# Optimization experiments

Measured on AMD Instinct MI355X. Metric: run time of the kernel, lower is better.

## Reference

```python
import jax, jax.numpy as jnp
import numpy as np

NEG_INF = -1e9  # matches torch masked_fill(-1000000000.0)


def setup_inputs() -> dict:
    key = jax.random.key(0)
    kv, kk, kq, km, kw, kb = jax.random.split(key, 6)
    B, Lq, Lk, D = 8, 1024, 4096, 1024  # Lq must equal D (transpose-then-merge quirk)
    v = jax.random.normal(kv, (B, Lk, D), dtype=jnp.float32)
    k = jax.random.normal(kk, (B, Lk, D), dtype=jnp.float32)
    q = jax.random.normal(kq, (B, Lq, D), dtype=jnp.float32)
    mask = jax.random.randint(km, (B, Lq, Lk), 0, 2) > 0  # bool, True = masked out
    W_merge = jax.random.normal(kw, (D, D), dtype=jnp.float32) / np.sqrt(D)
    b_merge = jax.random.normal(kb, (D,), dtype=jnp.float32) * 0.02
    return {"v": v, "k": k, "q": q, "mask": mask, "W_merge": W_merge, "b_merge": b_merge}


def reference(v, k, q, mask, W_merge, b_merge):
    d_k = q.shape[-1]
    scale = 1.0 / jnp.sqrt(jnp.asarray(d_k, dtype=q.dtype))
    # scores: [B, Lq, Lk]
    scores = jnp.einsum('bqd,bkd->bqk', q, k) * scale
    scores = jnp.where(mask, jnp.asarray(NEG_INF, dtype=scores.dtype), scores)
    att_map = jax.nn.softmax(scores, axis=-1)  # dropout = identity in eval
    atted = jnp.einsum('bqk,bkd->bqd', att_map, v)  # [B, Lq, D]
    atted = jnp.swapaxes(atted, -1, -2)  # [B, D, Lq]; Lq == hid_dim
    # nn.Linear: y = x @ W^T + b
    return jnp.einsum('bdl,ol->bdo', atted, W_merge) + b_merge
```

## Files before the change

### kernel.cpp

```cpp
#include <hip/hip_runtime.h>
#include <stdint.h>

typedef __attribute__((ext_vector_type(4))) float f32x4;
typedef __attribute__((ext_vector_type(8))) short bf16x8;
typedef __attribute__((ext_vector_type(4))) short bf16x4v;
typedef __attribute__((ext_vector_type(4))) unsigned int u32x4;

#define NBATCH 8
#define LQS    1024
#define LKS    4096
#define DDIM   1024
#define QKSCALE 0.03125f
#define NEGINF -1000000000.0f
#define BK 64

__device__ __forceinline__ short f2bf(float x) {
    unsigned u = __builtin_bit_cast(unsigned, x);
    unsigned r = (u + 0x7fffu + ((u >> 16) & 1u)) >> 16;
    return (short)r;
}

__device__ __forceinline__ bf16x8 cvt8(const float* f) {
    const u32x4* u = (const u32x4*)f;
    const u32x4 a = u[0], b = u[1];
    union { unsigned w[4]; bf16x8 v; } c;
    c.w[0] = __builtin_amdgcn_perm(a[1], a[0], 0x07060302u);
    c.w[1] = __builtin_amdgcn_perm(a[3], a[2], 0x07060302u);
    c.w[2] = __builtin_amdgcn_perm(b[1], b[0], 0x07060302u);
    c.w[3] = __builtin_amdgcn_perm(b[3], b[2], 0x07060302u);
    return c.v;
}

__device__ __forceinline__ void g2l16(const void* g, void* lds) {
    __builtin_amdgcn_global_load_lds(
        (const __attribute__((address_space(1))) unsigned int*)g,
        (__attribute__((address_space(3))) unsigned int*)lds,
        16, 0, 0);
}

__device__ __forceinline__ int xcd_swz(int bid, int nwg) {
    return (bid & 7) * (nwg >> 3) + (bid >> 3);
}

__global__ void detect_kernel(const unsigned char* __restrict__ mb,
                              int* __restrict__ flags) {
    if (threadIdx.x != 0 || blockIdx.x != 0) return;
    int is_i32 = 1;
    for (int i = 0; i < 256; ++i) {
        if ((i & 3) != 0 && mb[i] != 0) { is_i32 = 0; break; }
    }
    flags[0] = is_i32;
}

__global__ __launch_bounds__(256) void cvt_kernel(
    const float* __restrict__ src, short* __restrict__ dst, int n8) {
    const int stride = gridDim.x * 256;
    for (int i = blockIdx.x * 256 + threadIdx.x; i < n8; i += stride)
        ((bf16x8*)dst)[i] = cvt8(src + (size_t)i * 8);
}

__global__ __launch_bounds__(256) void add2_kernel(
    const float* __restrict__ p0, const float* __restrict__ p1,
    short* __restrict__ dst, int n8) {
    const int stride = gridDim.x * 256;
    for (int i = blockIdx.x * 256 + threadIdx.x; i < n8; i += stride) {
        const f32x4 a0 = ((const f32x4*)p0)[2 * i];
        const f32x4 a1 = ((const f32x4*)p0)[2 * i + 1];
        const f32x4 b0 = ((const f32x4*)p1)[2 * i];
        const f32x4 b1 = ((const f32x4*)p1)[2 * i + 1];
        bf16x8 r;
#pragma unroll
        for (int j = 0; j < 4; ++j) r[j]     = f2bf(a0[j] + b0[j]);
#pragma unroll
        for (int j = 0; j < 4; ++j) r[4 + j] = f2bf(a1[j] + b1[j]);
        ((bf16x8*)dst)[i] = r;
    }
}

__global__ __launch_bounds__(256) void transv_kernel(
    const float* __restrict__ V, short* __restrict__ VT) {
    __shared__ short LDSt[64 * 72];
    const int tid = threadIdx.x;
    const int cb  = blockIdx.x >> 10;
    const int t   = blockIdx.x & 1023;
    const int kt  = t >> 4, dt = t & 15;
    const int k0  = kt * 64, d0 = dt * 64;
    const float* Vb  = V  + (size_t)cb * LKS * DDIM;
    short*       VTb = VT + (size_t)cb * ((size_t)DDIM * LKS);

    const int r  = tid >> 4;
    const int cp = (tid & 15) * 4;
#pragma unroll
    for (int rr = 0; rr < 4; ++rr) {
        const int row = rr * 16 + r;
        const f32x4 v = *(const f32x4*)(Vb + (size_t)(k0 + row) * DDIM + d0 + cp);
#pragma unroll
        for (int i = 0; i < 4; ++i) LDSt[(cp + i) * 72 + row] = f2bf(v[i]);
    }
    __syncthreads();
    const int dr = tid >> 2;
    const int kq = (tid & 3) * 16;
    const bf16x8 o0 = *(const bf16x8*)&LDSt[dr * 72 + kq];
    const bf16x8 o1 = *(const bf16x8*)&LDSt[dr * 72 + kq + 8];
    short* dst = VTb + (size_t)(d0 + dr) * LKS + k0 + kq;
    *(bf16x8*)dst       = o0;
    *(bf16x8*)(dst + 8) = o1;
}

__device__ __forceinline__ void stage_half(const short* gbase, int ld,
                                           short* ldshalf, int tid) {
    const int r0 = tid >> 3;
    const int gc = (tid & 7) ^ (r0 & 7);
    const short* s0 = gbase + (size_t)r0 * ld + gc * 8;
    const short* s1 = gbase + (size_t)(r0 + 64) * ld + gc * 8;
    g2l16(s0, ldshalf + (tid & 0x1C0) * 8);
    g2l16(s1, ldshalf + 4096 + (tid & 0x1C0) * 8);
}

__device__ __forceinline__ bf16x8 rdfrag(const short* lds, int base, int r, int c) {
    return *(const bf16x8*)&lds[base + r * 64 + ((c ^ (r & 7)) << 3)];
}

#define MFMA16(d, a, b) d = __builtin_amdgcn_mfma_f32_16x16x32_bf16(a, b, d, 0, 0, 0)

#define PHASE(MF0, STAGE, TAIL)                                             \
    {                                                                       \
        bf16x8 a00 = rdfrag(lds, aBase, (MF0) * 16 + lo, g);                \
        bf16x8 a01 = rdfrag(lds, aBase, (MF0) * 16 + lo, 4 + g);            \
        bf16x8 a10 = rdfrag(lds, aBase, (MF0) * 16 + 16 + lo, g);          \
        bf16x8 a11 = rdfrag(lds, aBase, (MF0) * 16 + 16 + lo, 4 + g);      \
        STAGE;                                                              \
        asm volatile("s_barrier" ::: "memory");                             \
        __builtin_amdgcn_s_setprio(1);                                      \
        _Pragma("unroll")                                                   \
        for (int nf = 0; nf < 4; ++nf) {                                    \
            MFMA16(acc[(MF0)][nf], a00, bfr[nf][0]);                        \
            MFMA16(acc[(MF0)][nf], a01, bfr[nf][1]);                        \
            MFMA16(acc[(MF0) + 1][nf], a10, bfr[nf][0]);                    \
            MFMA16(acc[(MF0) + 1][nf], a11, bfr[nf][1]);                    \
        }                                                                   \
        __builtin_amdgcn_s_setprio(0);                                      \
        TAIL;                                                               \
        asm volatile("s_barrier" ::: "memory");                             \
    }

template <int EPI>
__device__ __forceinline__ void gemm8p_body(
    const short* __restrict__ A, int lda,
    const short* __restrict__ B, int ldb,
    void* __restrict__ C, int ldc,
    const float* __restrict__ bias,
    int m0, int n0, int NK, float scale, short* lds) {

    const int tid = threadIdx.x;
    const int w = tid >> 6, lane = tid & 63;
    const int lo = lane & 15, g = lane >> 4;
    const int wr = w >> 2, wc = w & 3;

    const short* gA0 = A + (size_t)m0 * lda;
    const short* gA1 = A + (size_t)(m0 + 128) * lda;
    const short* gB0 = B + (size_t)n0 * ldb;
    const short* gB1 = B + (size_t)(n0 + 128) * ldb;

    f32x4 acc[8][4];
#pragma unroll
    for (int mf = 0; mf < 8; ++mf)
#pragma unroll
        for (int nf = 0; nf < 4; ++nf) acc[mf][nf] = (f32x4){0.f, 0.f, 0.f, 0.f};

    stage_half(gA0, lda, lds + 0,     tid);
    stage_half(gA1, lda, lds + 8192,  tid);
    stage_half(gB0, ldb, lds + 16384, tid);
    stage_half(gB1, ldb, lds + 24576, tid);
    stage_half(gB0 + BK, ldb, lds + 32768 + 16384, tid);
    stage_half(gB1 + BK, ldb, lds + 32768 + 24576, tid);
    asm volatile("s_waitcnt vmcnt(4)" ::: "memory");
    asm volatile("s_barrier" ::: "memory");

    for (int kt = 0; kt < NK; ++kt) {
        const int cb = (kt & 1) << 15;
        const int ob = cb ^ 32768;
        const int aBase = cb + wr * 8192;
        const int bBase = cb + 16384 + (wc >> 1) * 8192;
        const int brow  = (wc & 1) * 64;
        const int kA = (kt + 1) * BK, kB = (kt + 2) * BK;
        const bool doA = (kt + 1) < NK, doB = (kt + 2) < NK;

        bf16x8 bfr[4][2];
#pragma unroll
        for (int nf = 0; nf < 4; ++nf) {
            bfr[nf][0] = rdfrag(lds, bBase, brow + nf * 16 + lo, g);
            bfr[nf][1] = rdfrag(lds, bBase, brow + nf * 16 + lo, 4 + g);
        }
        PHASE(0, if (doA) stage_half(gA0 + kA, lda, lds + ob, tid), )
        PHASE(2, if (doA) stage_half(gA1 + kA, lda, lds + ob + 8192, tid), )
        PHASE(4, if (doB) stage_half(gB0 + kB, ldb, lds + cb + 16384, tid), )
        PHASE(6, if (doB) stage_half(gB1 + kB, ldb, lds + cb + 24576, tid),
                 {
                     if (doB) { asm volatile("s_waitcnt vmcnt(4)" ::: "memory"); }
                     else     { asm volatile("s_waitcnt vmcnt(0)" ::: "memory"); }
                 })
    }

#pragma unroll
    for (int nf = 0; nf < 4; ++nf) {
        const int col = n0 + wc * 64 + nf * 16 + lo;
        float bv = 0.f;
        if constexpr (EPI == 2) bv = bias[col];
#pragma unroll
        for (int mf = 0; mf < 8; ++mf) {
#pragma unroll
            for (int rr = 0; rr < 4; ++rr) {
                const size_t oa =
                    (size_t)(m0 + wr * 128 + mf * 16 + g * 4 + rr) * ldc + col;
                if constexpr (EPI == 0)      ((float*)C)[oa] = acc[mf][nf][rr] * scale;
                else if constexpr (EPI == 1) ((short*)C)[oa] = f2bf(acc[mf][nf][rr]);
                else                         ((float*)C)[oa] = acc[mf][nf][rr] + bv;
            }
        }
    }
}

__global__ __launch_bounds__(512, 2) void gemm1_kernel(
    const short* __restrict__ Qb, const short* __restrict__ Kb,
    float* __restrict__ S) {
    __shared__ __align__(16) short lds[65536];
    const int bid = xcd_swz(blockIdx.x, gridDim.x);
    const int cb = bid >> 6;
    const int t  = bid & 63;
    gemm8p_body<0>(Qb + (size_t)cb * LQS * DDIM, DDIM,
                   Kb + (size_t)cb * LKS * DDIM, DDIM,
                   S + (size_t)cb * ((size_t)LQS * LKS), LKS, nullptr,
                   (t >> 4) * 256, (t & 15) * 256, DDIM / BK, QKSCALE, lds);
}

__global__ __launch_bounds__(512, 2) void gemm2_kernel(
    const short* __restrict__ VT, const short* __restrict__ Pd,
    float* __restrict__ Cpart, int nb) {
    __shared__ __align__(16) short lds[65536];
    const int bid = xcd_swz(blockIdx.x, gridDim.x);
    const int cb = bid >> 5;
    const int t  = (bid >> 1) & 15;
    const int s  = bid & 1;
    float* Cp = Cpart + (size_t)s * nb * (1 << 20) + (size_t)cb * (1 << 20);
    gemm8p_body<0>(VT + (size_t)cb * ((size_t)DDIM * LKS) + s * 2048, LKS,
                   Pd + (size_t)cb * ((size_t)LQS * LKS) + s * 2048, LKS,
                   Cp, LQS, nullptr,
                   (t >> 2) * 256, (t & 3) * 256, 2048 / BK, 1.f, lds);
}

__global__ __launch_bounds__(512, 2) void merge_kernel(
    const short* __restrict__ attedT, const short* __restrict__ Wb,
    const float* __restrict__ bias, float* __restrict__ out) {
    __shared__ __align__(16) short lds[65536];
    const int bid = xcd_swz(blockIdx.x, gridDim.x);
    const int mt = bid >> 2;
    const int nt = bid & 3;
    gemm8p_body<2>(attedT, DDIM, Wb, DDIM, out, DDIM, bias,
                   mt * 256, nt * 256, DDIM / BK, 1.f, lds);
}

__global__ __launch_bounds__(256) void softmax_kernel(
    const float* __restrict__ S, short* __restrict__ Pd,
    const void* __restrict__ mask, const int* __restrict__ flags, int c0) {
    __shared__ float red[4];
    const int tid = threadIdx.x, w = tid >> 6, lane = tid & 63;
    const int cb = blockIdx.x >> 10;
    const int q  = blockIdx.x & 1023;
    const int mflag = flags[0];

    const float* Srow = S + ((size_t)cb * LQS + q) * LKS;
    const size_t roff = ((size_t)(c0 + cb) * LQS + q) * LKS;

    float sc[16];
#pragma unroll
    for (int j = 0; j < 4; ++j) {
        const f32x4 sv = ((const f32x4*)Srow)[j * 256 + tid];
        int m0, m1, m2, m3;
        if (mflag) {
            const int4 mv = ((const int4*)((const int*)mask + roff))[j * 256 + tid];
            m0 = mv.x; m1 = mv.y; m2 = mv.z; m3 = mv.w;
        } else {
            const uchar4 mv = ((const uchar4*)((const unsigned char*)mask + roff))[j * 256 + tid];
            m0 = mv.x; m1 = mv.y; m2 = mv.z; m3 = mv.w;
        }
        sc[j * 4 + 0] = m0 ? NEGINF : sv[0];
        sc[j * 4 + 1] = m1 ? NEGINF : sv[1];
        sc[j * 4 + 2] = m2 ? NEGINF : sv[2];
        sc[j * 4 + 3] = m3 ? NEGINF : sv[3];
    }

    float lm = -INFINITY;
#pragma unroll
    for (int i = 0; i < 16; ++i) lm = fmaxf(lm, sc[i]);
#pragma unroll
    for (int off = 1; off < 64; off <<= 1) lm = fmaxf(lm, __shfl_xor(lm, off));
    if (lane == 0) red[w] = lm;
    __syncthreads();
    const float m = fmaxf(fmaxf(red[0], red[1]), fmaxf(red[2], red[3]));

    float p[16], ls = 0.f;
#pragma unroll
    for (int i = 0; i < 16; ++i) { p[i] = __expf(sc[i] - m); ls += p[i]; }
#pragma unroll
    for (int off = 1; off < 64; off <<= 1) ls += __shfl_xor(ls, off);
    __syncthreads();
    if (lane == 0) red[w] = ls;
    __syncthreads();
    const float inv = 1.f / (red[0] + red[1] + red[2] + red[3]);

    short* Prow = Pd + ((size_t)cb * LQS + q) * LKS;
#pragma unroll
    for (int j = 0; j < 4; ++j) {
        bf16x4v pv;
#pragma unroll
        for (int i = 0; i < 4; ++i) pv[i] = f2bf(p[j * 4 + i] * inv);
        ((bf16x4v*)Prow)[j * 256 + tid] = pv;
    }
}

extern "C" void kernel_launch(void* const* d_in, const int* in_sizes, int n_in,
                              void* d_out, int out_size, void* d_ws, size_t ws_size,
                              hipStream_t stream) {
    const float* v    = (const float*)d_in[0];
    const float* k    = (const float*)d_in[1];
    const float* q    = (const float*)d_in[2];
    const void*  mask = d_in[3];
    const float* Wm   = (const float*)d_in[4];
    const float* bias = (const float*)d_in[5];
    float* out = (float*)d_out;

    const size_t base = 4096 + (2ull << 20);
    int nb = 0;
    for (int cand = 8; cand >= 1; cand >>= 1)
        if (base + (size_t)cand * (36ull << 20) <= ws_size) { nb = cand; break; }
    if (!nb) return;

    int*   flags = (int*)d_ws;
    short* Wb    = (short*)((char*)d_ws + 4096);
    char*  ar    = (char*)d_ws + base;
    float* Sbuf   = (float*)ar;
    short* VTbuf  = (short*)(ar + ((size_t)nb << 24));
    short* attedT = (short*)(ar + ((size_t)nb << 24) + ((size_t)nb << 23));
    short* Qb     = (short*)(ar + ((size_t)nb << 24) + ((size_t)nb << 23) + ((size_t)nb << 21));
    short* Kb     = (short*)(ar + ((size_t)nb << 24) + ((size_t)nb << 23) + 2 * ((size_t)nb << 21));
    short* Pd     = Kb;
    float* Cpart  = Sbuf;

    hipLaunchKernelGGL(detect_kernel, dim3(1), dim3(64), 0, stream,
                       (const unsigned char*)mask, flags);
    hipLaunchKernelGGL(cvt_kernel, dim3(512), dim3(256), 0, stream,
                       Wm, Wb, (int)(DDIM * DDIM / 8));

    for (int c0 = 0; c0 < NBATCH; c0 += nb) {
        const float* vc = v + (size_t)c0 * LKS * DDIM;
        const float* kc = k + (size_t)c0 * LKS * DDIM;
        const float* qc = q + (size_t)c0 * LQS * DDIM;
        float*       oc = out + (size_t)c0 * DDIM * LQS;

        hipLaunchKernelGGL(cvt_kernel, dim3(1024), dim3(256), 0, stream,
                           qc, Qb, nb * (LQS * DDIM / 8));
        hipLaunchKernelGGL(cvt_kernel, dim3(2048), dim3(256), 0, stream,
                           kc, Kb, nb * (LKS * DDIM / 8));
        hipLaunchKernelGGL(transv_kernel, dim3(nb * 1024), dim3(256), 0, stream,
                           vc, VTbuf);
        hipLaunchKernelGGL(gemm1_kernel, dim3(nb * 64), dim3(512), 0, stream,
                           Qb, Kb, Sbuf);
        hipLaunchKernelGGL(softmax_kernel, dim3(nb * 1024), dim3(256), 0, stream,
                           Sbuf, Pd, mask, flags, c0);
        hipLaunchKernelGGL(gemm2_kernel, dim3(nb * 32), dim3(512), 0, stream,
                           VTbuf, Pd, Cpart, nb);
        hipLaunchKernelGGL(add2_kernel, dim3(1024), dim3(256), 0, stream,
                           Cpart, Cpart + (size_t)nb * (1 << 20), attedT,
                           nb * (1 << 17));
        hipLaunchKernelGGL(merge_kernel, dim3(nb * 16), dim3(512), 0, stream,
                           attedT, Wb, bias, oc);
    }
}
```

Measured before the change: 367.1 us.

## Store scores as bf16, drop split-K in PV GEMM, add 256x128 GEMM tile

```diff
diff --git a/kernel.cpp b/kernel.cpp
--- a/kernel.cpp
+++ b/kernel.cpp
@@ -18,6 +18,10 @@
     unsigned u = __builtin_bit_cast(unsigned, x);
     unsigned r = (u + 0x7fffu + ((u >> 16) & 1u)) >> 16;
     return (short)r;
+}
+__device__ __forceinline__ float bf2f(short s) {
+    unsigned u = ((unsigned)(unsigned short)s) << 16;
+    return __builtin_bit_cast(float, u);
 }
 
 __device__ __forceinline__ bf16x8 cvt8(const float* f) {
@@ -57,24 +61,6 @@
     const int stride = gridDim.x * 256;
     for (int i = blockIdx.x * 256 + threadIdx.x; i < n8; i += stride)
         ((bf16x8*)dst)[i] = cvt8(src + (size_t)i * 8);
-}
-
-__global__ __launch_bounds__(256) void add2_kernel(
-    const float* __restrict__ p0, const float* __restrict__ p1,
-    short* __restrict__ dst, int n8) {
-    const int stride = gridDim.x * 256;
-    for (int i = blockIdx.x * 256 + threadIdx.x; i < n8; i += stride) {
-        const f32x4 a0 = ((const f32x4*)p0)[2 * i];
-        const f32x4 a1 = ((const f32x4*)p0)[2 * i + 1];
-        const f32x4 b0 = ((const f32x4*)p1)[2 * i];
-        const f32x4 b1 = ((const f32x4*)p1)[2 * i + 1];
-        bf16x8 r;
-#pragma unroll
-        for (int j = 0; j < 4; ++j) r[j]     = f2bf(a0[j] + b0[j]);
-#pragma unroll
-        for (int j = 0; j < 4; ++j) r[4 + j] = f2bf(a1[j] + b1[j]);
-        ((bf16x8*)dst)[i] = r;
-    }
 }
 
 __global__ __launch_bounds__(256) void transv_kernel(
@@ -215,53 +201,130 @@
                     (size_t)(m0 + wr * 128 + mf * 16 + g * 4 + rr) * ldc + col;
                 if constexpr (EPI == 0)      ((float*)C)[oa] = acc[mf][nf][rr] * scale;
                 else if constexpr (EPI == 1) ((short*)C)[oa] = f2bf(acc[mf][nf][rr]);
-                else                         ((float*)C)[oa] = acc[mf][nf][rr] + bv;
+                else if constexpr (EPI == 2) ((float*)C)[oa] = acc[mf][nf][rr] + bv;
+                else                         ((short*)C)[oa] = f2bf(acc[mf][nf][rr] * scale);
             }
         }
     }
 }
 
+template <int EPI>
+__device__ __forceinline__ void gemm8p_n128(
+    const short* __restrict__ A, int lda,
+    const short* __restrict__ B, int ldb,
+    void* __restrict__ C, int ldc,
+    const float* __restrict__ bias,
+    int m0, int n0, int NK, float scale, short* lds) {
+
+    const int tid = threadIdx.x;
+    const int w = tid >> 6, lane = tid & 63;
+    const int lo = lane & 15, g = lane >> 4;
+    const int wr = w >> 1, wc = w & 1;
+
+    const short* gA0 = A + (size_t)m0 * lda;
+    const short* gA1 = A + (size_t)(m0 + 128) * lda;
+    const short* gB0 = B + (size_t)n0 * ldb;
+
+    f32x4 acc[4][4];
+#pragma unroll
+    for (int mf = 0; mf < 4; ++mf)
+#pragma unroll
+        for (int nf = 0; nf < 4; ++nf) acc[mf][nf] = (f32x4){0.f, 0.f, 0.f, 0.f};
+
+    stage_half(gA0, lda, lds + 0,    tid);
+    stage_half(gA1, lda, lds + 8192, tid);
+    stage_half(gB0, ldb, lds + 16384, tid);
+    stage_half(gB0 + BK, ldb, lds + 24576 + 16384, tid);
+    asm volatile("s_waitcnt vmcnt(2)" ::: "memory");
+    asm volatile("s_barrier" ::: "memory");
+
+    for (int kt = 0; kt < NK; ++kt) {
+        const int cbuf = (kt & 1) * 24576;
+        const int obuf = cbuf ^ 24576;
+        const int aBase = cbuf + (wr >> 1) * 8192 + (wr & 1) * 4096;
+        const int bBase = cbuf + 16384 + wc * 4096;
+        const int kA = (kt + 1) * BK, kB = (kt + 2) * BK;
+        const bool doA = (kt + 1) < NK, doB = (kt + 2) < NK;
+
+        bf16x8 bfr[4][2];
+#pragma unroll
+        for (int nf = 0; nf < 4; ++nf) {
+            bfr[nf][0] = rdfrag(lds, bBase, nf * 16 + lo, g);
+            bfr[nf][1] = rdfrag(lds, bBase, nf * 16 + lo, 4 + g);
+        }
+        PHASE(0, {
+            if (doA) {
+                stage_half(gA0 + kA, lda, lds + obuf, tid);
+                stage_half(gA1 + kA, lda, lds + obuf + 8192, tid);
+            }
+        }, )
+        PHASE(2, {
+            if (doB) stage_half(gB0 + kB, ldb, lds + cbuf + 16384, tid);
+        }, {
+            if (doB) { asm volatile("s_waitcnt vmcnt(2)" ::: "memory"); }
+            else     { asm volatile("s_waitcnt vmcnt(0)" ::: "memory"); }
+        })
+    }
+
+#pragma unroll
+    for (int nf = 0; nf < 4; ++nf) {
+        const int col = n0 + wc * 64 + nf * 16 + lo;
+        float bv = 0.f;
+        if constexpr (EPI == 2) bv = bias[col];
+#pragma unroll
+        for (int mf = 0; mf < 4; ++mf) {
+#pragma unroll
+            for (int rr = 0; rr < 4; ++rr) {
+                const size_t oa =
+                    (size_t)(m0 + wr * 64 + mf * 16 + g * 4 + rr) * ldc + col;
+                if constexpr (EPI == 0)      ((float*)C)[oa] = acc[mf][nf][rr] * scale;
+                else if constexpr (EPI == 1) ((short*)C)[oa] = f2bf(acc[mf][nf][rr]);
+                else if constexpr (EPI == 2) ((float*)C)[oa] = acc[mf][nf][rr] + bv;
+                else                         ((short*)C)[oa] = f2bf(acc[mf][nf][rr] * scale);
+            }
+        }
+    }
+}
+
 __global__ __launch_bounds__(512, 2) void gemm1_kernel(
     const short* __restrict__ Qb, const short* __restrict__ Kb,
-    float* __restrict__ S) {
+    short* __restrict__ Sb) {
     __shared__ __align__(16) short lds[65536];
     const int bid = xcd_swz(blockIdx.x, gridDim.x);
     const int cb = bid >> 6;
     const int t  = bid & 63;
-    gemm8p_body<0>(Qb + (size_t)cb * LQS * DDIM, DDIM,
+    gemm8p_body<3>(Qb + (size_t)cb * LQS * DDIM, DDIM,
                    Kb + (size_t)cb * LKS * DDIM, DDIM,
-                   S + (size_t)cb * ((size_t)LQS * LKS), LKS, nullptr,
+                   Sb + (size_t)cb * ((size_t)LQS * LKS), LKS, nullptr,
                    (t >> 4) * 256, (t & 15) * 256, DDIM / BK, QKSCALE, lds);
 }
 
 __global__ __launch_bounds__(512, 2) void gemm2_kernel(
     const short* __restrict__ VT, const short* __restrict__ Pd,
-    float* __restrict__ Cpart, int nb) {
-    __shared__ __align__(16) short lds[65536];
+    short* __restrict__ attedT) {
+    __shared__ __align__(16) short lds[49152];
     const int bid = xcd_swz(blockIdx.x, gridDim.x);
     const int cb = bid >> 5;
-    const int t  = (bid >> 1) & 15;
-    const int s  = bid & 1;
-    float* Cp = Cpart + (size_t)s * nb * (1 << 20) + (size_t)cb * (1 << 20);
-    gemm8p_body<0>(VT + (size_t)cb * ((size_t)DDIM * LKS) + s * 2048, LKS,
-                   Pd + (size_t)cb * ((size_t)LQS * LKS) + s * 2048, LKS,
-                   Cp, LQS, nullptr,
-                   (t >> 2) * 256, (t & 3) * 256, 2048 / BK, 1.f, lds);
+    const int t  = bid & 31;
+    gemm8p_n128<1>(VT + (size_t)cb * ((size_t)DDIM * LKS), LKS,
+                   Pd + (size_t)cb * ((size_t)LQS * LKS), LKS,
+                   attedT + (size_t)cb * ((size_t)DDIM * LQS), LQS, nullptr,
+                   (t >> 3) * 256, (t & 7) * 128, LKS / BK, 1.f, lds);
 }
 
 __global__ __launch_bounds__(512, 2) void merge_kernel(
     const short* __restrict__ attedT, const short* __restrict__ Wb,
     const float* __restrict__ bias, float* __restrict__ out) {
-    __shared__ __align__(16) short lds[65536];
+    __shared__ __align__(16) short lds[49152];
     const int bid = xcd_swz(blockIdx.x, gridDim.x);
-    const int mt = bid >> 2;
-    const int nt = bid & 3;
-    gemm8p_body<2>(attedT, DDIM, Wb, DDIM, out, DDIM, bias,
-                   mt * 256, nt * 256, DDIM / BK, 1.f, lds);
+    const int mt = bid >> 3;
+    const int nt = bid & 7;
+    gemm8p_n128<2>(attedT, DDIM, Wb, DDIM, out, DDIM, bias,
+                   mt * 256, nt * 128, DDIM / BK, 1.f, lds);
 }
 
 __global__ __launch_bounds__(256) void softmax_kernel(
-    const float* __restrict__ S, short* __restrict__ Pd,
+    const short* __restrict__ Sb, short* __restrict__ Pd,
     const void* __restrict__ mask, const int* __restrict__ flags, int c0) {
     __shared__ float red[4];
     const int tid = threadIdx.x, w = tid >> 6, lane = tid & 63;
@@ -269,25 +332,30 @@
     const int q  = blockIdx.x & 1023;
     const int mflag = flags[0];
 
-    const float* Srow = S + ((size_t)cb * LQS + q) * LKS;
+    const short* Srow = Sb + ((size_t)cb * LQS + q) * LKS;
     const size_t roff = ((size_t)(c0 + cb) * LQS + q) * LKS;
+    const size_t m4   = roff >> 2;
 
     float sc[16];
 #pragma unroll
-    for (int j = 0; j < 4; ++j) {
-        const f32x4 sv = ((const f32x4*)Srow)[j * 256 + tid];
-        int m0, m1, m2, m3;
+    for (int j = 0; j < 2; ++j) {
+        const int i8 = j * 256 + tid;
+        const bf16x8 sv = ((const bf16x8*)Srow)[i8];
+        int mm[8];
         if (mflag) {
-            const int4 mv = ((const int4*)((const int*)mask + roff))[j * 256 + tid];
-            m0 = mv.x; m1 = mv.y; m2 = mv.z; m3 = mv.w;
+            const int4 a = ((const int4*)mask)[m4 + 2 * i8];
+            const int4 b = ((const int4*)mask)[m4 + 2 * i8 + 1];
+            mm[0] = a.x; mm[1] = a.y; mm[2] = a.z; mm[3] = a.w;
+            mm[4] = b.x; mm[5] = b.y; mm[6] = b.z; mm[7] = b.w;
         } else {
-            const uchar4 mv = ((const uchar4*)((const unsigned char*)mask + roff))[j * 256 + tid];
-            m0 = mv.x; m1 = mv.y; m2 = mv.z; m3 = mv.w;
+            const uchar4 a = ((const uchar4*)mask)[m4 + 2 * i8];
+            const uchar4 b = ((const uchar4*)mask)[m4 + 2 * i8 + 1];
+            mm[0] = a.x; mm[1] = a.y; mm[2] = a.z; mm[3] = a.w;
+            mm[4] = b.x; mm[5] = b.y; mm[6] = b.z; mm[7] = b.w;
         }
-        sc[j * 4 + 0] = m0 ? NEGINF : sv[0];
-        sc[j * 4 + 1] = m1 ? NEGINF : sv[1];
-        sc[j * 4 + 2] = m2 ? NEGINF : sv[2];
-        sc[j * 4 + 3] = m3 ? NEGINF : sv[3];
+#pragma unroll
+        for (int i = 0; i < 8; ++i)
+            sc[j * 8 + i] = mm[i] ? NEGINF : bf2f(sv[i]);
     }
 
     float lm = -INFINITY;
@@ -311,11 +379,11 @@
 
     short* Prow = Pd + ((size_t)cb * LQS + q) * LKS;
 #pragma unroll
-    for (int j = 0; j < 4; ++j) {
-        bf16x4v pv;
-#pragma unroll
-        for (int i = 0; i < 4; ++i) pv[i] = f2bf(p[j * 4 + i] * inv);
-        ((bf16x4v*)Prow)[j * 256 + tid] = pv;
+    for (int j = 0; j < 2; ++j) {
+        bf16x8 pv;
+#pragma unroll
+        for (int i = 0; i < 8; ++i) pv[i] = f2bf(p[j * 8 + i] * inv);
+        ((bf16x8*)Prow)[j * 256 + tid] = pv;
     }
 }
 
@@ -339,13 +407,12 @@
     int*   flags = (int*)d_ws;
     short* Wb    = (short*)((char*)d_ws + 4096);
     char*  ar    = (char*)d_ws + base;
-    float* Sbuf   = (float*)ar;
+    short* Sb     = (short*)ar;
     short* VTbuf  = (short*)(ar + ((size_t)nb << 24));
     short* attedT = (short*)(ar + ((size_t)nb << 24) + ((size_t)nb << 23));
     short* Qb     = (short*)(ar + ((size_t)nb << 24) + ((size_t)nb << 23) + ((size_t)nb << 21));
     short* Kb     = (short*)(ar + ((size_t)nb << 24) + ((size_t)nb << 23) + 2 * ((size_t)nb << 21));
     short* Pd     = Kb;
-    float* Cpart  = Sbuf;
 
     hipLaunchKernelGGL(detect_kernel, dim3(1), dim3(64), 0, stream,
                        (const unsigned char*)mask, flags);
@@ -365,15 +432,12 @@
         hipLaunchKernelGGL(transv_kernel, dim3(nb * 1024), dim3(256), 0, stream,
                            vc, VTbuf);
         hipLaunchKernelGGL(gemm1_kernel, dim3(nb * 64), dim3(512), 0, stream,
-                           Qb, Kb, Sbuf);
+                           Qb, Kb, Sb);
         hipLaunchKernelGGL(softmax_kernel, dim3(nb * 1024), dim3(256), 0, stream,
-                           Sbuf, Pd, mask, flags, c0);
+                           Sb, Pd, mask, flags, c0);
         hipLaunchKernelGGL(gemm2_kernel, dim3(nb * 32), dim3(512), 0, stream,
-                           VTbuf, Pd, Cpart, nb);
-        hipLaunchKernelGGL(add2_kernel, dim3(1024), dim3(256), 0, stream,
-                           Cpart, Cpart + (size_t)nb * (1 << 20), attedT,
-                           nb * (1 << 17));
-        hipLaunchKernelGGL(merge_kernel, dim3(nb * 16), dim3(512), 0, stream,
+                           VTbuf, Pd, attedT);
+        hipLaunchKernelGGL(merge_kernel, dim3(nb * 32), dim3(512), 0, stream,
                            attedT, Wb, bias, oc);
     }
 }
```

Result: faster. 332.9 us (-9.3%).
